# Kernel tuning notes

Measured on AMD Instinct MI355X. Metric: run time of the kernel, lower is better.

Reference implementation:

```python
import jax, jax.numpy as jnp
import numpy as np

B, S, D, F, H, E = 4, 1024, 512, 2048, 8, 8
LN_EPS = 1e-5


def setup_inputs() -> dict:
    key = jax.random.key(0)
    ks = jax.random.split(key, 8)
    sd = 1.0 / np.sqrt(D)
    return {
        'x': jax.random.normal(ks[0], (B, S, D), jnp.float32),
        'in_proj_w': jax.random.normal(ks[1], (3 * D, D), jnp.float32) * sd,
        'in_proj_b': jnp.zeros((3 * D,), jnp.float32),
        'out_proj_w': jax.random.normal(ks[2], (D, D), jnp.float32) * sd,
        'out_proj_b': jnp.zeros((D,), jnp.float32),
        'ln1_g': jnp.ones((D,), jnp.float32),
        'ln1_b': jnp.zeros((D,), jnp.float32),
        'ln2_g': jnp.ones((D,), jnp.float32),
        'ln2_b': jnp.zeros((D,), jnp.float32),
        'router_w': jax.random.normal(ks[3], (D, E), jnp.float32) * sd,
        'wi': jax.random.normal(ks[4], (E, D, F), jnp.float32) * sd,
        'wo': jax.random.normal(ks[5], (E, F, D), jnp.float32) * (1.0 / np.sqrt(F)),
        'expert_capacity': 256,
    }


def _layernorm(x, g, b):
    mu = jnp.mean(x, axis=-1, keepdims=True)
    var = jnp.var(x, axis=-1, keepdims=True)
    return (x - mu) * jax.lax.rsqrt(var + LN_EPS) * g + b


def _mha(x, in_w, in_b, out_w, out_b):
    # torch nn.MultiheadAttention, batch_first, self-attention, no mask
    qkv = x @ in_w.T + in_b                         # [B,S,3D]
    q, k, v = jnp.split(qkv, 3, axis=-1)
    hd = D // H

    def heads(t):
        return t.reshape(B, S, H, hd).transpose(0, 2, 1, 3)  # [B,H,S,hd]

    q, k, v = heads(q), heads(k), heads(v)
    scores = jnp.einsum('bhqd,bhkd->bhqk', q, k) / np.sqrt(hd)
    attn = jax.nn.softmax(scores, axis=-1)
    o = jnp.einsum('bhqk,bhkd->bhqd', attn, v)
    o = o.transpose(0, 2, 1, 3).reshape(B, S, D)
    return o @ out_w.T + out_b


def _router(x, router_w, capacity):
    # Switch-style top-1 router with per-(batch,expert) capacity
    logits = x.astype(jnp.float32) @ router_w       # [B,S,E]
    probs = jax.nn.softmax(logits, axis=-1)
    idx = jnp.argmax(probs, axis=-1)                # [B,S]
    one_hot = jax.nn.one_hot(idx, E, dtype=probs.dtype)
    pos = jnp.cumsum(one_hot, axis=1)               # position within each expert queue
    keep = one_hot * (pos <= capacity).astype(probs.dtype)
    expert_mask = keep * probs                      # dispatch mask scaled by router prob
    return expert_mask, probs, logits


def reference(x, in_proj_w, in_proj_b, out_proj_w, out_proj_b,
              ln1_g, ln1_b, ln2_g, ln2_b, router_w, wi, wo, expert_capacity):
    # self-attention block (post-norm)
    residual = x
    a = _mha(x, in_proj_w, in_proj_b, out_proj_w, out_proj_b)
    h = _layernorm(residual + a, ln1_g, ln1_b)

    # sparse MoE FFN
    expert_mask, _, router_logits = _router(h, router_w, expert_capacity)
    residual = h
    moe = jnp.zeros_like(h)
    for e in range(E):  # fixed small expert loop; masked-dense == gather/FFN/scatter
        y = jax.nn.gelu(h @ wi[e], approximate=False) @ wo[e]
        moe = moe + expert_mask[..., e:e + 1] * y

    out = _layernorm(residual + moe, ln2_g, ln2_b)
    return out, router_logits, expert_mask
```

## Files before the change

### kernel.cpp

```cpp
#include <hip/hip_runtime.h>
#include <math.h>

#define SEQ 1024
#define NTOK 4096
#define DM 512
#define FF 2048
#define NE 8

typedef __attribute__((ext_vector_type(8))) short bf16x8;
typedef __attribute__((ext_vector_type(4))) float f32x4;

__device__ __forceinline__ short f2bf(float f) {
  unsigned u = __float_as_uint(f);
  unsigned r = (u + 0x7FFFu + ((u >> 16) & 1u)) >> 16;
  return (short)r;
}
__device__ __forceinline__ float bf2f(short h) {
  return __uint_as_float(((unsigned)(unsigned short)h) << 16);
}

#define GLOAD_LDS16(g, l) __builtin_amdgcn_global_load_lds( \
    (const __attribute__((address_space(1))) void*)(g),     \
    (__attribute__((address_space(3))) void*)(l), 16, 0, 0)

__global__ __launch_bounds__(256) void split3_kernel(
    const float* __restrict__ x, short* __restrict__ xh, short* __restrict__ xl,
    const float* __restrict__ w1, short* __restrict__ w1h, short* __restrict__ w1l,
    const float* __restrict__ w2, short* __restrict__ w2h, short* __restrict__ w2l) {
  const int bid = blockIdx.x;
  const float* src; short* hi; short* lo; size_t off;
  if (bid < 1024)      { src = x;  hi = xh;  lo = xl;  off = (size_t)bid * 2048; }
  else if (bid < 1408) { src = w1; hi = w1h; lo = w1l; off = (size_t)(bid - 1024) * 2048; }
  else                 { src = w2; hi = w2h; lo = w2l; off = (size_t)(bid - 1408) * 2048; }
  const size_t base = off + threadIdx.x * 8;
  float4 v0 = *reinterpret_cast<const float4*>(src + base);
  float4 v1 = *reinterpret_cast<const float4*>(src + base + 4);
  short h[8]; short l[8];
  float v[8] = {v0.x, v0.y, v0.z, v0.w, v1.x, v1.y, v1.z, v1.w};
#pragma unroll
  for (int i = 0; i < 8; ++i) {
    h[i] = f2bf(v[i]);
    l[i] = f2bf(v[i] - bf2f(h[i]));
  }
  *reinterpret_cast<short4*>(hi + base)     = make_short4(h[0], h[1], h[2], h[3]);
  *reinterpret_cast<short4*>(hi + base + 4) = make_short4(h[4], h[5], h[6], h[7]);
  *reinterpret_cast<short4*>(lo + base)     = make_short4(l[0], l[1], l[2], l[3]);
  *reinterpret_cast<short4*>(lo + base + 4) = make_short4(l[4], l[5], l[6], l[7]);
}

template<int BNF>
__global__ __launch_bounds__(256) void gemm_split(const short* __restrict__ Ah, const short* __restrict__ Al,
    const short* __restrict__ Bh, const short* __restrict__ Bl,
    const float* __restrict__ bias, const float* __restrict__ resid, float* __restrict__ C,
    int N, int K) {
  constexpr int BN = 32 * BNF;
  __shared__ __align__(16) short AsH[128 * 32];
  __shared__ __align__(16) short AsL[128 * 32];
  __shared__ __align__(16) short BsH[BN * 32];
  __shared__ __align__(16) short BsL[BN * 32];
  const int n0 = blockIdx.x * BN, m0 = blockIdx.y * 128;
  const int tid = threadIdx.x;
  const int lane = tid & 63, w = tid >> 6;
  const int quad = lane >> 4, l15 = lane & 15;
  const int wm = (w & 1) * 64, wn = (w >> 1) * 16 * BNF;
  const int sr = tid >> 2, sc = (tid & 3) * 8;
  const short* Ahp = Ah + (size_t)(m0 + sr) * K;
  const short* Alp = Al + (size_t)(m0 + sr) * K;
  const short* Bhp = Bh + (size_t)(n0 + sr) * K;
  const short* Blp = Bl + (size_t)(n0 + sr) * K;
  f32x4 acc[4][BNF];
#pragma unroll
  for (int i = 0; i < 4; ++i)
#pragma unroll
    for (int j = 0; j < BNF; ++j) acc[i][j] = (f32x4){0.f, 0.f, 0.f, 0.f};
  for (int kt = 0; kt < K; kt += 32) {
    GLOAD_LDS16(Ahp + kt + sc,                  &AsH[tid * 8]);
    GLOAD_LDS16(Ahp + (size_t)64 * K + kt + sc, &AsH[2048 + tid * 8]);
    GLOAD_LDS16(Alp + kt + sc,                  &AsL[tid * 8]);
    GLOAD_LDS16(Alp + (size_t)64 * K + kt + sc, &AsL[2048 + tid * 8]);
    if (BNF >= 2 || tid < 128) {
      GLOAD_LDS16(Bhp + kt + sc,                &BsH[tid * 8]);
      GLOAD_LDS16(Blp + kt + sc,                &BsL[tid * 8]);
    }
    if (BNF == 4) {
      GLOAD_LDS16(Bhp + (size_t)64 * K + kt + sc, &BsH[2048 + tid * 8]);
      GLOAD_LDS16(Blp + (size_t)64 * K + kt + sc, &BsL[2048 + tid * 8]);
    }
    __syncthreads();
    bf16x8 ah[4], al[4], bh[BNF], bl[BNF];
#pragma unroll
    for (int i = 0; i < 4; ++i) {
      ah[i] = *reinterpret_cast<const bf16x8*>(&AsH[(wm + i * 16 + l15) * 32 + quad * 8]);
      al[i] = *reinterpret_cast<const bf16x8*>(&AsL[(wm + i * 16 + l15) * 32 + quad * 8]);
    }
#pragma unroll
    for (int j = 0; j < BNF; ++j) {
      bh[j] = *reinterpret_cast<const bf16x8*>(&BsH[(wn + j * 16 + l15) * 32 + quad * 8]);
      bl[j] = *reinterpret_cast<const bf16x8*>(&BsL[(wn + j * 16 + l15) * 32 + quad * 8]);
    }
#pragma unroll
    for (int i = 0; i < 4; ++i)
#pragma unroll
      for (int j = 0; j < BNF; ++j) {
        acc[i][j] = __builtin_amdgcn_mfma_f32_16x16x32_bf16(al[i], bh[j], acc[i][j], 0, 0, 0);
        acc[i][j] = __builtin_amdgcn_mfma_f32_16x16x32_bf16(ah[i], bl[j], acc[i][j], 0, 0, 0);
        acc[i][j] = __builtin_amdgcn_mfma_f32_16x16x32_bf16(ah[i], bh[j], acc[i][j], 0, 0, 0);
      }
    __syncthreads();
  }
#pragma unroll
  for (int i = 0; i < 4; ++i) {
#pragma unroll
    for (int reg = 0; reg < 4; ++reg) {
      const int row = m0 + wm + i * 16 + quad * 4 + reg;
#pragma unroll
      for (int j = 0; j < BNF; ++j) {
        const int col = n0 + wn + j * 16 + l15;
        float v = acc[i][j][reg] + bias[col];
        if (resid) v += resid[(size_t)row * N + col];
        C[(size_t)row * N + col] = v;
      }
    }
  }
}

__global__ __launch_bounds__(256) void gemm_split_qkv(const short* __restrict__ Ah, const short* __restrict__ Al,
    const short* __restrict__ Bh, const short* __restrict__ Bl, const float* __restrict__ bias,
    short* __restrict__ qkh, short* __restrict__ qkl, short* __restrict__ vh, short* __restrict__ vl) {
  const int K = DM;
  __shared__ __align__(16) short AsH[128 * 32];
  __shared__ __align__(16) short AsL[128 * 32];
  __shared__ __align__(16) short BsH[64 * 32];
  __shared__ __align__(16) short BsL[64 * 32];
  const int n0 = blockIdx.x * 64, m0 = blockIdx.y * 128;
  const int tid = threadIdx.x;
  const int lane = tid & 63, w = tid >> 6;
  const int quad = lane >> 4, l15 = lane & 15;
  const int wm = (w & 1) * 64, wn = (w >> 1) * 32;
  const int sr = tid >> 2, sc = (tid & 3) * 8;
  const short* Ahp = Ah + (size_t)(m0 + sr) * K;
  const short* Alp = Al + (size_t)(m0 + sr) * K;
  const short* Bhp = Bh + (size_t)(n0 + sr) * K;
  const short* Blp = Bl + (size_t)(n0 + sr) * K;
  f32x4 acc[4][2];
#pragma unroll
  for (int i = 0; i < 4; ++i)
#pragma unroll
    for (int j = 0; j < 2; ++j) acc[i][j] = (f32x4){0.f, 0.f, 0.f, 0.f};
  for (int kt = 0; kt < K; kt += 32) {
    GLOAD_LDS16(Ahp + kt + sc,                  &AsH[tid * 8]);
    GLOAD_LDS16(Ahp + (size_t)64 * K + kt + sc, &AsH[2048 + tid * 8]);
    GLOAD_LDS16(Alp + kt + sc,                  &AsL[tid * 8]);
    GLOAD_LDS16(Alp + (size_t)64 * K + kt + sc, &AsL[2048 + tid * 8]);
    GLOAD_LDS16(Bhp + kt + sc,                  &BsH[tid * 8]);
    GLOAD_LDS16(Blp + kt + sc,                  &BsL[tid * 8]);
    __syncthreads();
    bf16x8 ah[4], al[4], bh[2], bl[2];
#pragma unroll
    for (int i = 0; i < 4; ++i) {
      ah[i] = *reinterpret_cast<const bf16x8*>(&AsH[(wm + i * 16 + l15) * 32 + quad * 8]);
      al[i] = *reinterpret_cast<const bf16x8*>(&AsL[(wm + i * 16 + l15) * 32 + quad * 8]);
    }
#pragma unroll
    for (int j = 0; j < 2; ++j) {
      bh[j] = *reinterpret_cast<const bf16x8*>(&BsH[(wn + j * 16 + l15) * 32 + quad * 8]);
      bl[j] = *reinterpret_cast<const bf16x8*>(&BsL[(wn + j * 16 + l15) * 32 + quad * 8]);
    }
#pragma unroll
    for (int i = 0; i < 4; ++i)
#pragma unroll
      for (int j = 0; j < 2; ++j) {
        acc[i][j] = __builtin_amdgcn_mfma_f32_16x16x32_bf16(al[i], bh[j], acc[i][j], 0, 0, 0);
        acc[i][j] = __builtin_amdgcn_mfma_f32_16x16x32_bf16(ah[i], bl[j], acc[i][j], 0, 0, 0);
        acc[i][j] = __builtin_amdgcn_mfma_f32_16x16x32_bf16(ah[i], bh[j], acc[i][j], 0, 0, 0);
      }
    __syncthreads();
  }
  if (n0 < 1024) {
#pragma unroll
    for (int i = 0; i < 4; ++i) {
#pragma unroll
      for (int reg = 0; reg < 4; ++reg) {
        const int row = m0 + wm + i * 16 + quad * 4 + reg;
#pragma unroll
        for (int j = 0; j < 2; ++j) {
          const int col = n0 + wn + j * 16 + l15;
          float v = acc[i][j][reg] + bias[col];
          short hv = f2bf(v);
          size_t ad = (size_t)row * 1024 + col;
          qkh[ad] = hv;
          qkl[ad] = f2bf(v - bf2f(hv));
        }
      }
    }
  } else {
#pragma unroll
    for (int i = 0; i < 4; ++i) {
      const int row0 = m0 + wm + i * 16 + quad * 4;
      const int bb = row0 >> 10, s0 = row0 & 1023;
#pragma unroll
      for (int j = 0; j < 2; ++j) {
        const int col = n0 + wn + j * 16 + l15;
        const int c2 = col - 1024;
        const int hhd = c2 >> 6, d = c2 & 63;
        const float bc = bias[col];
        float v0 = acc[i][j][0] + bc, v1 = acc[i][j][1] + bc, v2 = acc[i][j][2] + bc, v3 = acc[i][j][3] + bc;
        short4 hv = make_short4(f2bf(v0), f2bf(v1), f2bf(v2), f2bf(v3));
        short4 lv = make_short4(f2bf(v0 - bf2f(hv.x)), f2bf(v1 - bf2f(hv.y)),
                                f2bf(v2 - bf2f(hv.z)), f2bf(v3 - bf2f(hv.w)));
        size_t ad = ((size_t)(bb * 8 + hhd) * 64 + d) * 1024 + s0;
        *reinterpret_cast<short4*>(vh + ad) = hv;
        *reinterpret_cast<short4*>(vl + ad) = lv;
      }
    }
  }
}

__global__ __launch_bounds__(256) void attn_mfma(const short* __restrict__ qkh, const short* __restrict__ qkl,
    const short* __restrict__ vth, const short* __restrict__ vtl,
    float* __restrict__ opart, float* __restrict__ ml) {
  const int qt = blockIdx.x, hh = blockIdx.y;
  const int b = blockIdx.z >> 1, ks = blockIdx.z & 1;
  __shared__ __align__(16) short Kh[4096], Kl[4096], Vh[4096], Vl[4096];
  const int tid = threadIdx.x;
  const int lane = tid & 63, w = tid >> 6;
  const int quad = lane >> 4, l15 = lane & 15;
  const int tok0 = b * SEQ + qt * 64;
  const int srow = tid >> 2, schunk = (tid & 3) * 8;
  bf16x8 qfh[2], qfl[2];
  {
    const size_t qa = (size_t)(tok0 + w * 16 + l15) * 1024 + hh * 64 + quad * 8;
    qfh[0] = *reinterpret_cast<const bf16x8*>(qkh + qa);
    qfh[1] = *reinterpret_cast<const bf16x8*>(qkh + qa + 32);
    qfl[0] = *reinterpret_cast<const bf16x8*>(qkl + qa);
    qfl[1] = *reinterpret_cast<const bf16x8*>(qkl + qa + 32);
  }
  f32x4 oacc[4];
  float m_run[4], l_run[4];
#pragma unroll
  for (int r = 0; r < 4; ++r) { oacc[r] = (f32x4){0.f, 0.f, 0.f, 0.f}; m_run[r] = -1e30f; l_run[r] = 0.f; }
  const size_t kbase = (size_t)(b * SEQ) * 1024 + 512 + hh * 64;
  const size_t vbase = (size_t)(b * 8 + hh) * 64 * 1024;
  for (int kc = ks * 8; kc < ks * 8 + 8; ++kc) {
    const size_t ka = kbase + (size_t)(kc * 64 + srow) * 1024 + schunk;
    GLOAD_LDS16(qkh + ka,      &Kh[tid * 8]);
    GLOAD_LDS16(qkh + ka + 32, &Kh[2048 + tid * 8]);
    GLOAD_LDS16(qkl + ka,      &Kl[tid * 8]);
    GLOAD_LDS16(qkl + ka + 32, &Kl[2048 + tid * 8]);
    const size_t va = vbase + (size_t)srow * 1024 + kc * 64 + schunk;
    GLOAD_LDS16(vth + va,      &Vh[tid * 8]);
    GLOAD_LDS16(vth + va + 32, &Vh[2048 + tid * 8]);
    GLOAD_LDS16(vtl + va,      &Vl[tid * 8]);
    GLOAD_LDS16(vtl + va + 32, &Vl[2048 + tid * 8]);
    __syncthreads();
    f32x4 s[4];
#pragma unroll
    for (int j = 0; j < 4; ++j) s[j] = (f32x4){0.f, 0.f, 0.f, 0.f};
#pragma unroll
    for (int kk = 0; kk < 2; ++kk)
#pragma unroll
      for (int j = 0; j < 4; ++j) {
        bf16x8 kfh = *reinterpret_cast<const bf16x8*>(&Kh[kk * 2048 + (j * 16 + l15) * 32 + quad * 8]);
        bf16x8 kfl = *reinterpret_cast<const bf16x8*>(&Kl[kk * 2048 + (j * 16 + l15) * 32 + quad * 8]);
        s[j] = __builtin_amdgcn_mfma_f32_16x16x32_bf16(qfl[kk], kfh, s[j], 0, 0, 0);
        s[j] = __builtin_amdgcn_mfma_f32_16x16x32_bf16(qfh[kk], kfl, s[j], 0, 0, 0);
        s[j] = __builtin_amdgcn_mfma_f32_16x16x32_bf16(qfh[kk], kfh, s[j], 0, 0, 0);
      }
    __syncthreads();
    float pv[4][4], alpha[4];
#pragma unroll
    for (int reg = 0; reg < 4; ++reg) {
      float mc = fmaxf(fmaxf(s[0][reg], s[1][reg]), fmaxf(s[2][reg], s[3][reg]));
#pragma unroll
      for (int msk = 1; msk < 16; msk <<= 1) mc = fmaxf(mc, __shfl_xor(mc, msk, 64));
      mc *= 0.125f;
      float mn = fmaxf(m_run[reg], mc);
      alpha[reg] = expf(m_run[reg] - mn);
      m_run[reg] = mn;
      float pl = 0.f;
#pragma unroll
      for (int j = 0; j < 4; ++j) { float pp = expf(s[j][reg] * 0.125f - mn); pv[j][reg] = pp; pl += pp; }
#pragma unroll
      for (int msk = 1; msk < 16; msk <<= 1) pl += __shfl_xor(pl, msk, 64);
      l_run[reg] = l_run[reg] * alpha[reg] + pl;
    }
#pragma unroll
    for (int j = 0; j < 4; ++j) {
      oacc[j][0] *= alpha[0]; oacc[j][1] *= alpha[1]; oacc[j][2] *= alpha[2]; oacc[j][3] *= alpha[3];
    }
#pragma unroll
    for (int j = 0; j < 4; ++j) {
      const int cad = (j >> 1) * 2048 + (j & 1) * 16 + l15;
#pragma unroll
      for (int reg = 0; reg < 4; ++reg) {
        const int ad = cad + (w * 16 + quad * 4 + reg) * 32;
        float p = pv[j][reg];
        short hp = f2bf(p);
        Kh[ad] = hp;
        Kl[ad] = f2bf(p - bf2f(hp));
      }
    }
#pragma unroll
    for (int kk = 0; kk < 2; ++kk) {
      bf16x8 pfh = *reinterpret_cast<const bf16x8*>(&Kh[kk * 2048 + (w * 16 + l15) * 32 + quad * 8]);
      bf16x8 pfl = *reinterpret_cast<const bf16x8*>(&Kl[kk * 2048 + (w * 16 + l15) * 32 + quad * 8]);
#pragma unroll
      for (int j = 0; j < 4; ++j) {
        bf16x8 vfh = *reinterpret_cast<const bf16x8*>(&Vh[kk * 2048 + (j * 16 + l15) * 32 + quad * 8]);
        bf16x8 vfl = *reinterpret_cast<const bf16x8*>(&Vl[kk * 2048 + (j * 16 + l15) * 32 + quad * 8]);
        oacc[j] = __builtin_amdgcn_mfma_f32_16x16x32_bf16(pfl, vfh, oacc[j], 0, 0, 0);
        oacc[j] = __builtin_amdgcn_mfma_f32_16x16x32_bf16(pfh, vfl, oacc[j], 0, 0, 0);
        oacc[j] = __builtin_amdgcn_mfma_f32_16x16x32_bf16(pfh, vfh, oacc[j], 0, 0, 0);
      }
    }
    __syncthreads();
  }
  float* op = opart + (size_t)ks * 2097152;
#pragma unroll
  for (int reg = 0; reg < 4; ++reg) {
    const int rloc = w * 16 + quad * 4 + reg;
#pragma unroll
    for (int j = 0; j < 4; ++j)
      op[(size_t)(tok0 + rloc) * 512 + hh * 64 + j * 16 + l15] = oacc[j][reg];
    if (l15 == 0) {
      size_t mli = (((size_t)ks * 32 + b * 8 + hh) * 1024 + qt * 64 + rloc) * 2;
      ml[mli] = m_run[reg];
      ml[mli + 1] = l_run[reg];
    }
  }
}

__global__ __launch_bounds__(64) void combine_attn(const float* __restrict__ opart, const float* __restrict__ ml,
    short* __restrict__ oh, short* __restrict__ ol) {
  const int t = blockIdx.x;
  const int b = t >> 10, s = t & 1023;
  const int tid = threadIdx.x;
#pragma unroll
  for (int hh = 0; hh < 8; ++hh) {
    size_t mli = (((size_t)(b * 8 + hh)) * 1024 + s) * 2;
    float m0 = ml[mli], l0 = ml[mli + 1];
    float m1 = ml[65536 + mli], l1 = ml[65536 + mli + 1];
    float mm = fmaxf(m0, m1);
    float a0 = expf(m0 - mm), a1 = expf(m1 - mm);
    float inv = 1.f / (l0 * a0 + l1 * a1);
    size_t ad = (size_t)t * 512 + hh * 64 + tid;
    float v = (opart[ad] * a0 + opart[2097152 + ad] * a1) * inv;
    short hv = f2bf(v);
    oh[ad] = hv;
    ol[ad] = f2bf(v - bf2f(hv));
  }
}

__global__ __launch_bounds__(64) void ln_router(const float* __restrict__ r1,
    const float* __restrict__ g, const float* __restrict__ bta, const float* __restrict__ rw,
    float* __restrict__ h, float* __restrict__ rlog, float* __restrict__ probs, int* __restrict__ am) {
  const int t = blockIdx.x, tid = threadIdx.x;
  const size_t base = (size_t)t * DM + tid * 8;
  float4 v0 = *reinterpret_cast<const float4*>(r1 + base);
  float4 v1 = *reinterpret_cast<const float4*>(r1 + base + 4);
  float s = v0.x+v0.y+v0.z+v0.w + v1.x+v1.y+v1.z+v1.w;
  float q = v0.x*v0.x+v0.y*v0.y+v0.z*v0.z+v0.w*v0.w + v1.x*v1.x+v1.y*v1.y+v1.z*v1.z+v1.w*v1.w;
#pragma unroll
  for (int m = 1; m < 64; m <<= 1) { s += __shfl_xor(s, m, 64); q += __shfl_xor(q, m, 64); }
  float mean = s * (1.0f/512.0f);
  float var = q * (1.0f/512.0f) - mean * mean;
  float rs = rsqrtf(var + 1e-5f);
  float4 g0 = *reinterpret_cast<const float4*>(g + tid*8);
  float4 g1 = *reinterpret_cast<const float4*>(g + tid*8 + 4);
  float4 b0 = *reinterpret_cast<const float4*>(bta + tid*8);
  float4 b1 = *reinterpret_cast<const float4*>(bta + tid*8 + 4);
  float hv[8];
  hv[0] = (v0.x-mean)*rs*g0.x+b0.x; hv[1] = (v0.y-mean)*rs*g0.y+b0.y;
  hv[2] = (v0.z-mean)*rs*g0.z+b0.z; hv[3] = (v0.w-mean)*rs*g0.w+b0.w;
  hv[4] = (v1.x-mean)*rs*g1.x+b1.x; hv[5] = (v1.y-mean)*rs*g1.y+b1.y;
  hv[6] = (v1.z-mean)*rs*g1.z+b1.z; hv[7] = (v1.w-mean)*rs*g1.w+b1.w;
  *reinterpret_cast<float4*>(h + base)     = make_float4(hv[0], hv[1], hv[2], hv[3]);
  *reinterpret_cast<float4*>(h + base + 4) = make_float4(hv[4], hv[5], hv[6], hv[7]);
  float lg[8] = {0.f,0.f,0.f,0.f,0.f,0.f,0.f,0.f};
  const float* rwp = rw + tid * 64;
#pragma unroll
  for (int r = 0; r < 8; ++r) {
    float4 w0 = *reinterpret_cast<const float4*>(rwp + r * 8);
    float4 w1 = *reinterpret_cast<const float4*>(rwp + r * 8 + 4);
    float hr = hv[r];
    lg[0] += hr * w0.x; lg[1] += hr * w0.y; lg[2] += hr * w0.z; lg[3] += hr * w0.w;
    lg[4] += hr * w1.x; lg[5] += hr * w1.y; lg[6] += hr * w1.z; lg[7] += hr * w1.w;
  }
#pragma unroll
  for (int m = 1; m < 64; m <<= 1) {
#pragma unroll
    for (int e = 0; e < 8; ++e) lg[e] += __shfl_xor(lg[e], m, 64);
  }
  int best = 0; float bv = lg[0];
#pragma unroll
  for (int e = 1; e < 8; ++e) if (lg[e] > bv) { bv = lg[e]; best = e; }
  float se = 0.f;
#pragma unroll
  for (int e = 0; e < 8; ++e) se += expf(lg[e] - bv);
  float inv = 1.f / se;
  if (tid < 8) {
    rlog[t * 8 + tid] = lg[tid];
    probs[t * 8 + tid] = expf(lg[tid] - bv) * inv;
  }
  if (tid == 0) am[t] = best;
}

__global__ __launch_bounds__(64) void ln2_kernel(const float* __restrict__ x, const float* __restrict__ add,
    const int* __restrict__ pos, const int* __restrict__ capp,
    const float* __restrict__ g, const float* __restrict__ bta, float* __restrict__ y) {
  const int t = blockIdx.x, tid = threadIdx.x;
  const size_t base = (size_t)t * DM + tid * 8;
  float4 v0 = *reinterpret_cast<const float4*>(x + base);
  float4 v1 = *reinterpret_cast<const float4*>(x + base + 4);
  if (pos[t] <= *capp) {
    float4 a0 = *reinterpret_cast<const float4*>(add + base);
    float4 a1 = *reinterpret_cast<const float4*>(add + base + 4);
    v0.x += a0.x; v0.y += a0.y; v0.z += a0.z; v0.w += a0.w;
    v1.x += a1.x; v1.y += a1.y; v1.z += a1.z; v1.w += a1.w;
  }
  float s = v0.x+v0.y+v0.z+v0.w + v1.x+v1.y+v1.z+v1.w;
  float q = v0.x*v0.x+v0.y*v0.y+v0.z*v0.z+v0.w*v0.w + v1.x*v1.x+v1.y*v1.y+v1.z*v1.z+v1.w*v1.w;
#pragma unroll
  for (int m = 1; m < 64; m <<= 1) { s += __shfl_xor(s, m, 64); q += __shfl_xor(q, m, 64); }
  float mean = s * (1.0f/512.0f);
  float var = q * (1.0f/512.0f) - mean * mean;
  float rs = rsqrtf(var + 1e-5f);
  float4 g0 = *reinterpret_cast<const float4*>(g + tid*8);
  float4 g1 = *reinterpret_cast<const float4*>(g + tid*8 + 4);
  float4 b0 = *reinterpret_cast<const float4*>(bta + tid*8);
  float4 b1 = *reinterpret_cast<const float4*>(bta + tid*8 + 4);
  float4 o0 = make_float4((v0.x-mean)*rs*g0.x+b0.x, (v0.y-mean)*rs*g0.y+b0.y,
                          (v0.z-mean)*rs*g0.z+b0.z, (v0.w-mean)*rs*g0.w+b0.w);
  float4 o1 = make_float4((v1.x-mean)*rs*g1.x+b1.x, (v1.y-mean)*rs*g1.y+b1.y,
                          (v1.z-mean)*rs*g1.z+b1.z, (v1.w-mean)*rs*g1.w+b1.w);
  *reinterpret_cast<float4*>(y + base) = o0;
  *reinterpret_cast<float4*>(y + base + 4) = o1;
}

__global__ __launch_bounds__(256) void scan_kernel(const int* __restrict__ am, const float* __restrict__ probs,
    const int* __restrict__ capp, float* __restrict__ emask, int* __restrict__ pos, int* __restrict__ cnt) {
  const int bx = blockIdx.x;
  const int b = bx >> 3, e = bx & 7;
  const int tid = threadIdx.x;
  const int cap = *capp;
  __shared__ int arr[256];
  const int s_base = tid * 4;
  int f[4], incl[4];
  int c = 0;
#pragma unroll
  for (int i = 0; i < 4; ++i) {
    f[i] = (am[b * SEQ + s_base + i] == e) ? 1 : 0;
    c += f[i]; incl[i] = c;
  }
  arr[tid] = c;
  __syncthreads();
  for (int off = 1; off < 256; off <<= 1) {
    int v = (tid >= off) ? arr[tid - off] : 0;
    __syncthreads();
    arr[tid] += v;
    __syncthreads();
  }
  int excl = arr[tid] - c;
  int tot = arr[255];
#pragma unroll
  for (int i = 0; i < 4; ++i) {
    int token = b * SEQ + s_base + i;
    int p = excl + incl[i];
    bool kept = f[i] && (p <= cap);
    emask[(size_t)token * NE + e] = kept ? probs[token * NE + e] : 0.f;
    if (f[i]) pos[token] = p;
  }
  if (tid == 0) cnt[bx] = (tot < cap) ? tot : cap;
}

__global__ __launch_bounds__(256) void transpose2_bf16(const float* __restrict__ wi, short* __restrict__ wi_t,
    const float* __restrict__ wo, short* __restrict__ wo_t) {
  __shared__ float T[32][33];
  const int z = blockIdx.z;
  const float* W; short* Wt; int K, N, k0, n0;
  if (z < 8) { W = wi + (size_t)z * DM * FF;      Wt = wi_t + (size_t)z * DM * FF;
               K = DM; N = FF; k0 = blockIdx.y * 32; n0 = blockIdx.x * 32; }
  else       { W = wo + (size_t)(z - 8) * FF * DM; Wt = wo_t + (size_t)(z - 8) * FF * DM;
               K = FF; N = DM; k0 = blockIdx.x * 32; n0 = blockIdx.y * 32; }
  const int r = threadIdx.x >> 3, c4 = (threadIdx.x & 7) * 4;
  float4 v = *reinterpret_cast<const float4*>(&W[(size_t)(k0 + r) * N + n0 + c4]);
  T[r][c4+0] = v.x; T[r][c4+1] = v.y; T[r][c4+2] = v.z; T[r][c4+3] = v.w;
  __syncthreads();
  short4 o;
  o.x = f2bf(T[c4+0][r]); o.y = f2bf(T[c4+1][r]); o.z = f2bf(T[c4+2][r]); o.w = f2bf(T[c4+3][r]);
  *reinterpret_cast<short4*>(&Wt[(size_t)(n0 + r) * K + k0 + c4]) = o;
}

__global__ __launch_bounds__(128) void gather_kernel(const float* __restrict__ h, const int* __restrict__ am,
    const int* __restrict__ pos, const int* __restrict__ capp, const int* __restrict__ cnt,
    const float* __restrict__ probs, short* __restrict__ Gb, int* __restrict__ tok, float* __restrict__ mscale) {
  const int t = blockIdx.x;
  const int b = t >> 10;
  const int e = am[t];
  const int p = pos[t];
  if (p > *capp) return;
  int off = 0;
  for (int b2 = 0; b2 < b; ++b2) off += cnt[b2 * 8 + e];
  const int slot = off + p - 1;
  const int idx = e * 1024 + slot;
  if (threadIdx.x == 0) { tok[idx] = t; mscale[idx] = probs[t * NE + e]; }
  float4 v = *reinterpret_cast<const float4*>(h + (size_t)t * DM + threadIdx.x * 4);
  short4 o; o.x = f2bf(v.x); o.y = f2bf(v.y); o.z = f2bf(v.z); o.w = f2bf(v.w);
  *reinterpret_cast<short4*>(Gb + (size_t)idx * DM + threadIdx.x * 4) = o;
}

__global__ __launch_bounds__(256) void ffn1_mfma(const short* __restrict__ Gb, const short* __restrict__ wi_t,
    short* __restrict__ mid, const int* __restrict__ cnt) {
  const int e = blockIdx.z;
  const int tot = cnt[e] + cnt[8 + e] + cnt[16 + e] + cnt[24 + e];
  const int m0 = blockIdx.y * 128;
  if (m0 >= tot) return;
  const int n0 = blockIdx.x * 128;
  __shared__ __align__(16) short As[128 * 32];
  __shared__ __align__(16) short Bs[128 * 32];
  const short* A = Gb + ((size_t)e * 1024 + m0) * DM;
  const short* B = wi_t + (size_t)e * FF * DM + (size_t)n0 * DM;
  const int tid = threadIdx.x;
  const int lane = tid & 63, w = tid >> 6;
  const int quad = lane >> 4, l15 = lane & 15;
  const int wm = (w & 1) * 64, wn = (w >> 1) * 64;
  const int sr = tid >> 2, sc = (tid & 3) * 8;
  f32x4 acc[4][4];
#pragma unroll
  for (int i = 0; i < 4; ++i)
#pragma unroll
    for (int j = 0; j < 4; ++j) acc[i][j] = (f32x4){0.f, 0.f, 0.f, 0.f};
  for (int kt = 0; kt < DM; kt += 32) {
    GLOAD_LDS16(A + (size_t)sr * DM + kt + sc,        &As[tid * 8]);
    GLOAD_LDS16(A + (size_t)(sr + 64) * DM + kt + sc, &As[2048 + tid * 8]);
    GLOAD_LDS16(B + (size_t)sr * DM + kt + sc,        &Bs[tid * 8]);
    GLOAD_LDS16(B + (size_t)(sr + 64) * DM + kt + sc, &Bs[2048 + tid * 8]);
    __syncthreads();
    bf16x8 a[4], b[4];
#pragma unroll
    for (int i = 0; i < 4; ++i) a[i] = *reinterpret_cast<const bf16x8*>(&As[(wm + i * 16 + l15) * 32 + quad * 8]);
#pragma unroll
    for (int j = 0; j < 4; ++j) b[j] = *reinterpret_cast<const bf16x8*>(&Bs[(wn + j * 16 + l15) * 32 + quad * 8]);
#pragma unroll
    for (int i = 0; i < 4; ++i)
#pragma unroll
      for (int j = 0; j < 4; ++j)
        acc[i][j] = __builtin_amdgcn_mfma_f32_16x16x32_bf16(a[i], b[j], acc[i][j], 0, 0, 0);
    __syncthreads();
  }
#pragma unroll
  for (int i = 0; i < 4; ++i) {
#pragma unroll
    for (int reg = 0; reg < 4; ++reg) {
      int row = m0 + wm + i * 16 + quad * 4 + reg;
      short* outr = mid + ((size_t)e * 1024 + row) * FF;
#pragma unroll
      for (int j = 0; j < 4; ++j) {
        float v = acc[i][j][reg];
        float gl = 0.5f * v * (1.f + erff(v * 0.70710678118654752f));
        outr[n0 + wn + j * 16 + l15] = f2bf(gl);
      }
    }
  }
}

__global__ __launch_bounds__(256) void ffn2_mfma(const short* __restrict__ mid, const short* __restrict__ wo_t,
    const int* __restrict__ tok, const float* __restrict__ mscale, const int* __restrict__ cnt,
    float* __restrict__ moebuf) {
  const int e = blockIdx.z;
  const int tot = cnt[e] + cnt[8 + e] + cnt[16 + e] + cnt[24 + e];
  const int m0 = blockIdx.y * 128;
  if (m0 >= tot) return;
  const int n0 = blockIdx.x * 64;
  __shared__ __align__(16) short As[128 * 32];
  __shared__ __align__(16) short Bs[64 * 32];
  const short* A = mid + ((size_t)e * 1024 + m0) * FF;
  const short* B = wo_t + (size_t)e * DM * FF + (size_t)n0 * FF;
  const int tid = threadIdx.x;
  const int lane = tid & 63, w = tid >> 6;
  const int quad = lane >> 4, l15 = lane & 15;
  const int wm = (w & 1) * 64, wn = (w >> 1) * 32;
  const int sr = tid >> 2, sc = (tid & 3) * 8;
  f32x4 acc[4][2];
#pragma unroll
  for (int i = 0; i < 4; ++i)
#pragma unroll
    for (int j = 0; j < 2; ++j) acc[i][j] = (f32x4){0.f, 0.f, 0.f, 0.f};
  for (int kt = 0; kt < FF; kt += 32) {
    GLOAD_LDS16(A + (size_t)sr * FF + kt + sc,        &As[tid * 8]);
    GLOAD_LDS16(A + (size_t)(sr + 64) * FF + kt + sc, &As[2048 + tid * 8]);
    GLOAD_LDS16(B + (size_t)sr * FF + kt + sc,        &Bs[tid * 8]);
    __syncthreads();
    bf16x8 a[4], b[2];
#pragma unroll
    for (int i = 0; i < 4; ++i) a[i] = *reinterpret_cast<const bf16x8*>(&As[(wm + i * 16 + l15) * 32 + quad * 8]);
#pragma unroll
    for (int j = 0; j < 2; ++j) b[j] = *reinterpret_cast<const bf16x8*>(&Bs[(wn + j * 16 + l15) * 32 + quad * 8]);
#pragma unroll
    for (int i = 0; i < 4; ++i)
#pragma unroll
      for (int j = 0; j < 2; ++j)
        acc[i][j] = __builtin_amdgcn_mfma_f32_16x16x32_bf16(a[i], b[j], acc[i][j], 0, 0, 0);
    __syncthreads();
  }
#pragma unroll
  for (int i = 0; i < 4; ++i) {
#pragma unroll
    for (int reg = 0; reg < 4; ++reg) {
      int slot = m0 + wm + i * 16 + quad * 4 + reg;
      if (slot < tot) {
        int idx = e * 1024 + slot;
        int t = tok[idx];
        float scv = mscale[idx];
        float* outr = moebuf + (size_t)t * DM + n0 + wn;
#pragma unroll
        for (int j = 0; j < 2; ++j) outr[j * 16 + l15] = scv * acc[i][j][reg];
      }
    }
  }
}

extern "C" void kernel_launch(void* const* d_in, const int* in_sizes, int n_in,
                              void* d_out, int out_size, void* d_ws, size_t ws_size,
                              hipStream_t stream) {
  const float* x     = (const float*)d_in[0];
  const float* in_w  = (const float*)d_in[1];
  const float* in_b  = (const float*)d_in[2];
  const float* out_w = (const float*)d_in[3];
  const float* out_b = (const float*)d_in[4];
  const float* ln1g  = (const float*)d_in[5];
  const float* ln1b  = (const float*)d_in[6];
  const float* ln2g  = (const float*)d_in[7];
  const float* ln2b  = (const float*)d_in[8];
  const float* rw    = (const float*)d_in[9];
  const float* wi    = (const float*)d_in[10];
  const float* wo    = (const float*)d_in[11];
  const int*   capp  = (const int*)d_in[12];

  float* ws = (float*)d_ws;
  short* qkh  = (short*)ws;
  short* qkl  = (short*)(ws + 2097152);
  short* vth  = (short*)(ws + 4194304);
  short* vtl  = (short*)(ws + 5242880);
  short* Gb16 = (short*)ws;
  short* wi_t = (short*)(ws + 2097152);
  float* moebuf = ws + 6291456;
  float* r1     = ws + 8388608;
  float* h      = ws + 10485760;
  float* probs  = ws + 12582912;
  short* wo_t   = (short*)(ws + 12615680);
  float* opart  = ws + 16809984;
  float* mlbuf  = ws + 16809984 + 4194304;
  short* mid16  = (short*)(ws + 16809984);
  float* mscale = ws + 25198592;
  int* am    = (int*)(ws + 25206784);
  int* pos   = am + NTOK;
  int* cnt   = pos + NTOK;
  int* tok   = cnt + 32;
  short* sAh = (short*)(ws + 25231360);
  short* sAl = sAh + 2097152;
  short* sBh = sAl + 2097152;
  short* sBl = sBh + 786432;
  short* sCh = sBl + 786432;
  short* sCl = sCh + 262144;

  float* out   = (float*)d_out;
  float* rlog  = out + 2097152;
  float* emask = rlog + 32768;

  split3_kernel<<<1536, 256, 0, stream>>>(x, sAh, sAl, in_w, sBh, sBl, out_w, sCh, sCl);
  gemm_split_qkv<<<dim3(24, 32), 256, 0, stream>>>(sAh, sAl, sBh, sBl, in_b, qkh, qkl, vth, vtl);
  attn_mfma<<<dim3(16, 8, 8), 256, 0, stream>>>(qkh, qkl, vth, vtl, opart, mlbuf);
  combine_attn<<<NTOK, 64, 0, stream>>>(opart, mlbuf, sAh, sAl);
  gemm_split<1><<<dim3(16, 32), 256, 0, stream>>>(sAh, sAl, sCh, sCl, out_b, x, r1, DM, DM);
  transpose2_bf16<<<dim3(64, 16, 16), 256, 0, stream>>>(wi, wi_t, wo, wo_t);
  ln_router<<<NTOK, 64, 0, stream>>>(r1, ln1g, ln1b, rw, h, rlog, probs, am);
  scan_kernel<<<32, 256, 0, stream>>>(am, probs, capp, emask, pos, cnt);
  gather_kernel<<<NTOK, 128, 0, stream>>>(h, am, pos, capp, cnt, probs, Gb16, tok, mscale);
  ffn1_mfma<<<dim3(16, 8, 8), 256, 0, stream>>>(Gb16, wi_t, mid16, cnt);
  ffn2_mfma<<<dim3(8, 8, 8), 256, 0, stream>>>(mid16, wo_t, tok, mscale, cnt, moebuf);
  ln2_kernel<<<NTOK, 64, 0, stream>>>(h, moebuf, pos, capp, ln2g, ln2b, out);
}
```

Measured before the change: 349.2 us.

## Double-buffer LDS tiles and shrink M-tiles in all GEMM kernels

Converts the QKV, out-projection and both MoE FFN GEMMs to a double-buffered LDS pipeline. The next K-slice is prefetched with global_load_lds while the current one feeds the MFMAs, leaving one barrier per iteration. M-tiles drop from 128 to 64 rows, which doubles the grid to fill more CUs and skips more empty expert slots. The cost is less operand reuse per block, more global traffic, and double the LDS footprint.

```diff
diff --git a/kernel.cpp b/kernel.cpp
--- a/kernel.cpp
+++ b/kernel.cpp
@@ -48,60 +48,52 @@
   *reinterpret_cast<short4*>(lo + base + 4) = make_short4(l[4], l[5], l[6], l[7]);
 }
 
-template<int BNF>
-__global__ __launch_bounds__(256) void gemm_split(const short* __restrict__ Ah, const short* __restrict__ Al,
+__global__ __launch_bounds__(256) void gemm_split_db(const short* __restrict__ Ah, const short* __restrict__ Al,
     const short* __restrict__ Bh, const short* __restrict__ Bl,
     const float* __restrict__ bias, const float* __restrict__ resid, float* __restrict__ C,
     int N, int K) {
-  constexpr int BN = 32 * BNF;
-  __shared__ __align__(16) short AsH[128 * 32];
-  __shared__ __align__(16) short AsL[128 * 32];
-  __shared__ __align__(16) short BsH[BN * 32];
-  __shared__ __align__(16) short BsL[BN * 32];
-  const int n0 = blockIdx.x * BN, m0 = blockIdx.y * 128;
+  __shared__ __align__(16) short AsH[2][2048], AsL[2][2048], BsH[2][2048], BsL[2][2048];
+  const int n0 = blockIdx.x * 64, m0 = blockIdx.y * 64;
   const int tid = threadIdx.x;
   const int lane = tid & 63, w = tid >> 6;
   const int quad = lane >> 4, l15 = lane & 15;
-  const int wm = (w & 1) * 64, wn = (w >> 1) * 16 * BNF;
+  const int wm = (w & 1) * 32, wn = (w >> 1) * 32;
   const int sr = tid >> 2, sc = (tid & 3) * 8;
-  const short* Ahp = Ah + (size_t)(m0 + sr) * K;
-  const short* Alp = Al + (size_t)(m0 + sr) * K;
-  const short* Bhp = Bh + (size_t)(n0 + sr) * K;
-  const short* Blp = Bl + (size_t)(n0 + sr) * K;
-  f32x4 acc[4][BNF];
-#pragma unroll
-  for (int i = 0; i < 4; ++i)
-#pragma unroll
-    for (int j = 0; j < BNF; ++j) acc[i][j] = (f32x4){0.f, 0.f, 0.f, 0.f};
+  const short* Ahp = Ah + (size_t)(m0 + sr) * K + sc;
+  const short* Alp = Al + (size_t)(m0 + sr) * K + sc;
+  const short* Bhp = Bh + (size_t)(n0 + sr) * K + sc;
+  const short* Blp = Bl + (size_t)(n0 + sr) * K + sc;
+  GLOAD_LDS16(Ahp, &AsH[0][tid * 8]);
+  GLOAD_LDS16(Alp, &AsL[0][tid * 8]);
+  GLOAD_LDS16(Bhp, &BsH[0][tid * 8]);
+  GLOAD_LDS16(Blp, &BsL[0][tid * 8]);
+  __syncthreads();
+  f32x4 acc[2][2];
+#pragma unroll
+  for (int i = 0; i < 2; ++i)
+#pragma unroll
+    for (int j = 0; j < 2; ++j) acc[i][j] = (f32x4){0.f, 0.f, 0.f, 0.f};
   for (int kt = 0; kt < K; kt += 32) {
-    GLOAD_LDS16(Ahp + kt + sc,                  &AsH[tid * 8]);
-    GLOAD_LDS16(Ahp + (size_t)64 * K + kt + sc, &AsH[2048 + tid * 8]);
-    GLOAD_LDS16(Alp + kt + sc,                  &AsL[tid * 8]);
-    GLOAD_LDS16(Alp + (size_t)64 * K + kt + sc, &AsL[2048 + tid * 8]);
-    if (BNF >= 2 || tid < 128) {
-      GLOAD_LDS16(Bhp + kt + sc,                &BsH[tid * 8]);
-      GLOAD_LDS16(Blp + kt + sc,                &BsL[tid * 8]);
-    }
-    if (BNF == 4) {
-      GLOAD_LDS16(Bhp + (size_t)64 * K + kt + sc, &BsH[2048 + tid * 8]);
-      GLOAD_LDS16(Blp + (size_t)64 * K + kt + sc, &BsL[2048 + tid * 8]);
-    }
-    __syncthreads();
-    bf16x8 ah[4], al[4], bh[BNF], bl[BNF];
-#pragma unroll
-    for (int i = 0; i < 4; ++i) {
-      ah[i] = *reinterpret_cast<const bf16x8*>(&AsH[(wm + i * 16 + l15) * 32 + quad * 8]);
-      al[i] = *reinterpret_cast<const bf16x8*>(&AsL[(wm + i * 16 + l15) * 32 + quad * 8]);
-    }
-#pragma unroll
-    for (int j = 0; j < BNF; ++j) {
-      bh[j] = *reinterpret_cast<const bf16x8*>(&BsH[(wn + j * 16 + l15) * 32 + quad * 8]);
-      bl[j] = *reinterpret_cast<const bf16x8*>(&BsL[(wn + j * 16 + l15) * 32 + quad * 8]);
-    }
-#pragma unroll
-    for (int i = 0; i < 4; ++i)
-#pragma unroll
-      for (int j = 0; j < BNF; ++j) {
+    const int cur = (kt >> 5) & 1;
+    if (kt + 32 < K) {
+      const int nxt = cur ^ 1;
+      GLOAD_LDS16(Ahp + kt + 32, &AsH[nxt][tid * 8]);
+      GLOAD_LDS16(Alp + kt + 32, &AsL[nxt][tid * 8]);
+      GLOAD_LDS16(Bhp + kt + 32, &BsH[nxt][tid * 8]);
+      GLOAD_LDS16(Blp + kt + 32, &BsL[nxt][tid * 8]);
+    }
+    bf16x8 ah[2], al[2], bh[2], bl[2];
+#pragma unroll
+    for (int i = 0; i < 2; ++i) {
+      ah[i] = *reinterpret_cast<const bf16x8*>(&AsH[cur][(wm + i * 16 + l15) * 32 + quad * 8]);
+      al[i] = *reinterpret_cast<const bf16x8*>(&AsL[cur][(wm + i * 16 + l15) * 32 + quad * 8]);
+      bh[i] = *reinterpret_cast<const bf16x8*>(&BsH[cur][(wn + i * 16 + l15) * 32 + quad * 8]);
+      bl[i] = *reinterpret_cast<const bf16x8*>(&BsL[cur][(wn + i * 16 + l15) * 32 + quad * 8]);
+    }
+#pragma unroll
+    for (int i = 0; i < 2; ++i)
+#pragma unroll
+      for (int j = 0; j < 2; ++j) {
         acc[i][j] = __builtin_amdgcn_mfma_f32_16x16x32_bf16(al[i], bh[j], acc[i][j], 0, 0, 0);
         acc[i][j] = __builtin_amdgcn_mfma_f32_16x16x32_bf16(ah[i], bl[j], acc[i][j], 0, 0, 0);
         acc[i][j] = __builtin_amdgcn_mfma_f32_16x16x32_bf16(ah[i], bh[j], acc[i][j], 0, 0, 0);
@@ -109,15 +101,14 @@
     __syncthreads();
   }
 #pragma unroll
-  for (int i = 0; i < 4; ++i) {
+  for (int i = 0; i < 2; ++i) {
 #pragma unroll
     for (int reg = 0; reg < 4; ++reg) {
       const int row = m0 + wm + i * 16 + quad * 4 + reg;
 #pragma unroll
-      for (int j = 0; j < BNF; ++j) {
+      for (int j = 0; j < 2; ++j) {
         const int col = n0 + wn + j * 16 + l15;
-        float v = acc[i][j][reg] + bias[col];
-        if (resid) v += resid[(size_t)row * N + col];
+        float v = acc[i][j][reg] + bias[col] + resid[(size_t)row * N + col];
         C[(size_t)row * N + col] = v;
       }
     }
@@ -128,46 +119,46 @@
     const short* __restrict__ Bh, const short* __restrict__ Bl, const float* __restrict__ bias,
     short* __restrict__ qkh, short* __restrict__ qkl, short* __restrict__ vh, short* __restrict__ vl) {
   const int K = DM;
-  __shared__ __align__(16) short AsH[128 * 32];
-  __shared__ __align__(16) short AsL[128 * 32];
-  __shared__ __align__(16) short BsH[64 * 32];
-  __shared__ __align__(16) short BsL[64 * 32];
-  const int n0 = blockIdx.x * 64, m0 = blockIdx.y * 128;
+  __shared__ __align__(16) short AsH[2][2048], AsL[2][2048], BsH[2][2048], BsL[2][2048];
+  const int n0 = blockIdx.x * 64, m0 = blockIdx.y * 64;
   const int tid = threadIdx.x;
   const int lane = tid & 63, w = tid >> 6;
   const int quad = lane >> 4, l15 = lane & 15;
-  const int wm = (w & 1) * 64, wn = (w >> 1) * 32;
+  const int wm = (w & 1) * 32, wn = (w >> 1) * 32;
   const int sr = tid >> 2, sc = (tid & 3) * 8;
-  const short* Ahp = Ah + (size_t)(m0 + sr) * K;
-  const short* Alp = Al + (size_t)(m0 + sr) * K;
-  const short* Bhp = Bh + (size_t)(n0 + sr) * K;
-  const short* Blp = Bl + (size_t)(n0 + sr) * K;
-  f32x4 acc[4][2];
-#pragma unroll
-  for (int i = 0; i < 4; ++i)
+  const short* Ahp = Ah + (size_t)(m0 + sr) * K + sc;
+  const short* Alp = Al + (size_t)(m0 + sr) * K + sc;
+  const short* Bhp = Bh + (size_t)(n0 + sr) * K + sc;
+  const short* Blp = Bl + (size_t)(n0 + sr) * K + sc;
+  GLOAD_LDS16(Ahp, &AsH[0][tid * 8]);
+  GLOAD_LDS16(Alp, &AsL[0][tid * 8]);
+  GLOAD_LDS16(Bhp, &BsH[0][tid * 8]);
+  GLOAD_LDS16(Blp, &BsL[0][tid * 8]);
+  __syncthreads();
+  f32x4 acc[2][2];
+#pragma unroll
+  for (int i = 0; i < 2; ++i)
 #pragma unroll
     for (int j = 0; j < 2; ++j) acc[i][j] = (f32x4){0.f, 0.f, 0.f, 0.f};
   for (int kt = 0; kt < K; kt += 32) {
-    GLOAD_LDS16(Ahp + kt + sc,                  &AsH[tid * 8]);
-    GLOAD_LDS16(Ahp + (size_t)64 * K + kt + sc, &AsH[2048 + tid * 8]);
-    GLOAD_LDS16(Alp + kt + sc,                  &AsL[tid * 8]);
-    GLOAD_LDS16(Alp + (size_t)64 * K + kt + sc, &AsL[2048 + tid * 8]);
-    GLOAD_LDS16(Bhp + kt + sc,                  &BsH[tid * 8]);
-    GLOAD_LDS16(Blp + kt + sc,                  &BsL[tid * 8]);
-    __syncthreads();
-    bf16x8 ah[4], al[4], bh[2], bl[2];
-#pragma unroll
-    for (int i = 0; i < 4; ++i) {
-      ah[i] = *reinterpret_cast<const bf16x8*>(&AsH[(wm + i * 16 + l15) * 32 + quad * 8]);
-      al[i] = *reinterpret_cast<const bf16x8*>(&AsL[(wm + i * 16 + l15) * 32 + quad * 8]);
-    }
-#pragma unroll
-    for (int j = 0; j < 2; ++j) {
-      bh[j] = *reinterpret_cast<const bf16x8*>(&BsH[(wn + j * 16 + l15) * 32 + quad * 8]);
-      bl[j] = *reinterpret_cast<const bf16x8*>(&BsL[(wn + j * 16 + l15) * 32 + quad * 8]);
-    }
-#pragma unroll
-    for (int i = 0; i < 4; ++i)
+    const int cur = (kt >> 5) & 1;
+    if (kt + 32 < K) {
+      const int nxt = cur ^ 1;
+      GLOAD_LDS16(Ahp + kt + 32, &AsH[nxt][tid * 8]);
+      GLOAD_LDS16(Alp + kt + 32, &AsL[nxt][tid * 8]);
+      GLOAD_LDS16(Bhp + kt + 32, &BsH[nxt][tid * 8]);
+      GLOAD_LDS16(Blp + kt + 32, &BsL[nxt][tid * 8]);
+    }
+    bf16x8 ah[2], al[2], bh[2], bl[2];
+#pragma unroll
+    for (int i = 0; i < 2; ++i) {
+      ah[i] = *reinterpret_cast<const bf16x8*>(&AsH[cur][(wm + i * 16 + l15) * 32 + quad * 8]);
+      al[i] = *reinterpret_cast<const bf16x8*>(&AsL[cur][(wm + i * 16 + l15) * 32 + quad * 8]);
+      bh[i] = *reinterpret_cast<const bf16x8*>(&BsH[cur][(wn + i * 16 + l15) * 32 + quad * 8]);
+      bl[i] = *reinterpret_cast<const bf16x8*>(&BsL[cur][(wn + i * 16 + l15) * 32 + quad * 8]);
+    }
+#pragma unroll
+    for (int i = 0; i < 2; ++i)
 #pragma unroll
       for (int j = 0; j < 2; ++j) {
         acc[i][j] = __builtin_amdgcn_mfma_f32_16x16x32_bf16(al[i], bh[j], acc[i][j], 0, 0, 0);
@@ -178,7 +169,7 @@
   }
   if (n0 < 1024) {
 #pragma unroll
-    for (int i = 0; i < 4; ++i) {
+    for (int i = 0; i < 2; ++i) {
 #pragma unroll
       for (int reg = 0; reg < 4; ++reg) {
         const int row = m0 + wm + i * 16 + quad * 4 + reg;
@@ -195,7 +186,7 @@
     }
   } else {
 #pragma unroll
-    for (int i = 0; i < 4; ++i) {
+    for (int i = 0; i < 2; ++i) {
       const int row0 = m0 + wm + i * 16 + quad * 4;
       const int bb = row0 >> 10, s0 = row0 & 1023;
 #pragma unroll
@@ -513,38 +504,45 @@
     short* __restrict__ mid, const int* __restrict__ cnt) {
   const int e = blockIdx.z;
   const int tot = cnt[e] + cnt[8 + e] + cnt[16 + e] + cnt[24 + e];
-  const int m0 = blockIdx.y * 128;
+  const int m0 = blockIdx.y * 64;
   if (m0 >= tot) return;
   const int n0 = blockIdx.x * 128;
-  __shared__ __align__(16) short As[128 * 32];
-  __shared__ __align__(16) short Bs[128 * 32];
-  const short* A = Gb + ((size_t)e * 1024 + m0) * DM;
-  const short* B = wi_t + (size_t)e * FF * DM + (size_t)n0 * DM;
+  __shared__ __align__(16) short As[2][2048];
+  __shared__ __align__(16) short Bs[2][4096];
   const int tid = threadIdx.x;
   const int lane = tid & 63, w = tid >> 6;
   const int quad = lane >> 4, l15 = lane & 15;
-  const int wm = (w & 1) * 64, wn = (w >> 1) * 64;
+  const int wn = w * 32;
   const int sr = tid >> 2, sc = (tid & 3) * 8;
-  f32x4 acc[4][4];
+  const short* Ap  = Gb + ((size_t)e * 1024 + m0 + sr) * DM + sc;
+  const short* Bp  = wi_t + (size_t)e * FF * DM + (size_t)(n0 + sr) * DM + sc;
+  const short* Bp2 = wi_t + (size_t)e * FF * DM + (size_t)(n0 + 64 + sr) * DM + sc;
+  GLOAD_LDS16(Ap,  &As[0][tid * 8]);
+  GLOAD_LDS16(Bp,  &Bs[0][tid * 8]);
+  GLOAD_LDS16(Bp2, &Bs[0][2048 + tid * 8]);
+  __syncthreads();
+  f32x4 acc[4][2];
 #pragma unroll
   for (int i = 0; i < 4; ++i)
 #pragma unroll
-    for (int j = 0; j < 4; ++j) acc[i][j] = (f32x4){0.f, 0.f, 0.f, 0.f};
+    for (int j = 0; j < 2; ++j) acc[i][j] = (f32x4){0.f, 0.f, 0.f, 0.f};
   for (int kt = 0; kt < DM; kt += 32) {
-    GLOAD_LDS16(A + (size_t)sr * DM + kt + sc,        &As[tid * 8]);
-    GLOAD_LDS16(A + (size_t)(sr + 64) * DM + kt + sc, &As[2048 + tid * 8]);
-    GLOAD_LDS16(B + (size_t)sr * DM + kt + sc,        &Bs[tid * 8]);
-    GLOAD_LDS16(B + (size_t)(sr + 64) * DM + kt + sc, &Bs[2048 + tid * 8]);
-    __syncthreads();
-    bf16x8 a[4], b[4];
-#pragma unroll
-    for (int i = 0; i < 4; ++i) a[i] = *reinterpret_cast<const bf16x8*>(&As[(wm + i * 16 + l15) * 32 + quad * 8]);
-#pragma unroll
-    for (int j = 0; j < 4; ++j) b[j] = *reinterpret_cast<const bf16x8*>(&Bs[(wn + j * 16 + l15) * 32 + quad * 8]);
+    const int cur = (kt >> 5) & 1;
+    if (kt + 32 < DM) {
+      const int nxt = cur ^ 1;
+      GLOAD_LDS16(Ap + kt + 32,  &As[nxt][tid * 8]);
+      GLOAD_LDS16(Bp + kt + 32,  &Bs[nxt][tid * 8]);
+      GLOAD_LDS16(Bp2 + kt + 32, &Bs[nxt][2048 + tid * 8]);
+    }
+    bf16x8 a[4], b[2];
+#pragma unroll
+    for (int i = 0; i < 4; ++i) a[i] = *reinterpret_cast<const bf16x8*>(&As[cur][(i * 16 + l15) * 32 + quad * 8]);
+#pragma unroll
+    for (int j = 0; j < 2; ++j) b[j] = *reinterpret_cast<const bf16x8*>(&Bs[cur][(wn + j * 16 + l15) * 32 + quad * 8]);
 #pragma unroll
     for (int i = 0; i < 4; ++i)
 #pragma unroll
-      for (int j = 0; j < 4; ++j)
+      for (int j = 0; j < 2; ++j)
         acc[i][j] = __builtin_amdgcn_mfma_f32_16x16x32_bf16(a[i], b[j], acc[i][j], 0, 0, 0);
     __syncthreads();
   }
@@ -552,10 +550,10 @@
   for (int i = 0; i < 4; ++i) {
 #pragma unroll
     for (int reg = 0; reg < 4; ++reg) {
-      int row = m0 + wm + i * 16 + quad * 4 + reg;
+      const int row = m0 + i * 16 + quad * 4 + reg;
       short* outr = mid + ((size_t)e * 1024 + row) * FF;
 #pragma unroll
-      for (int j = 0; j < 4; ++j) {
+      for (int j = 0; j < 2; ++j) {
         float v = acc[i][j][reg];
         float gl = 0.5f * v * (1.f + erff(v * 0.70710678118654752f));
         outr[n0 + wn + j * 16 + l15] = f2bf(gl);
@@ -569,49 +567,55 @@
     float* __restrict__ moebuf) {
   const int e = blockIdx.z;
   const int tot = cnt[e] + cnt[8 + e] + cnt[16 + e] + cnt[24 + e];
-  const int m0 = blockIdx.y * 128;
+  const int m0 = blockIdx.y * 64;
   if (m0 >= tot) return;
   const int n0 = blockIdx.x * 64;
-  __shared__ __align__(16) short As[128 * 32];
-  __shared__ __align__(16) short Bs[64 * 32];
-  const short* A = mid + ((size_t)e * 1024 + m0) * FF;
-  const short* B = wo_t + (size_t)e * DM * FF + (size_t)n0 * FF;
+  __shared__ __align__(16) short As[2][2048];
+  __shared__ __align__(16) short Bs[2][2048];
   const int tid = threadIdx.x;
   const int lane = tid & 63, w = tid >> 6;
   const int quad = lane >> 4, l15 = lane & 15;
-  const int wm = (w & 1) * 64, wn = (w >> 1) * 32;
+  const int wm = (w & 1) * 32, wn = (w >> 1) * 32;
   const int sr = tid >> 2, sc = (tid & 3) * 8;
-  f32x4 acc[4][2];
-#pragma unroll
-  for (int i = 0; i < 4; ++i)
+  const short* Ap = mid + ((size_t)e * 1024 + m0 + sr) * FF + sc;
+  const short* Bp = wo_t + (size_t)e * DM * FF + (size_t)(n0 + sr) * FF + sc;
+  GLOAD_LDS16(Ap, &As[0][tid * 8]);
+  GLOAD_LDS16(Bp, &Bs[0][tid * 8]);
+  __syncthreads();
+  f32x4 acc[2][2];
+#pragma unroll
+  for (int i = 0; i < 2; ++i)
 #pragma unroll
     for (int j = 0; j < 2; ++j) acc[i][j] = (f32x4){0.f, 0.f, 0.f, 0.f};
   for (int kt = 0; kt < FF; kt += 32) {
-    GLOAD_LDS16(A + (size_t)sr * FF + kt + sc,        &As[tid * 8]);
-    GLOAD_LDS16(A + (size_t)(sr + 64) * FF + kt + sc, &As[2048 + tid * 8]);
-    GLOAD_LDS16(B + (size_t)sr * FF + kt + sc,        &Bs[tid * 8]);
-    __syncthreads();
-    bf16x8 a[4], b[2];
-#pragma unroll
-    for (int i = 0; i < 4; ++i) a[i] = *reinterpret_cast<const bf16x8*>(&As[(wm + i * 16 + l15) * 32 + quad * 8]);
-#pragma unroll
-    for (int j = 0; j < 2; ++j) b[j] = *reinterpret_cast<const bf16x8*>(&Bs[(wn + j * 16 + l15) * 32 + quad * 8]);
-#pragma unroll
-    for (int i = 0; i < 4; ++i)
+    const int cur = (kt >> 5) & 1;
+    if (kt + 32 < FF) {
+      const int nxt = cur ^ 1;
+      GLOAD_LDS16(Ap + kt + 32, &As[nxt][tid * 8]);
+      GLOAD_LDS16(Bp + kt + 32, &Bs[nxt][tid * 8]);
+    }
+    bf16x8 a[2], b[2];
+#pragma unroll
+    for (int i = 0; i < 2; ++i) {
+      a[i] = *reinterpret_cast<const bf16x8*>(&As[cur][(wm + i * 16 + l15) * 32 + quad * 8]);
+      b[i] = *reinterpret_cast<const bf16x8*>(&Bs[cur][(wn + i * 16 + l15) * 32 + quad * 8]);
+    }
+#pragma unroll
+    for (int i = 0; i < 2; ++i)
 #pragma unroll
       for (int j = 0; j < 2; ++j)
         acc[i][j] = __builtin_amdgcn_mfma_f32_16x16x32_bf16(a[i], b[j], acc[i][j], 0, 0, 0);
     __syncthreads();
   }
 #pragma unroll
-  for (int i = 0; i < 4; ++i) {
+  for (int i = 0; i < 2; ++i) {
 #pragma unroll
     for (int reg = 0; reg < 4; ++reg) {
-      int slot = m0 + wm + i * 16 + quad * 4 + reg;
+      const int slot = m0 + wm + i * 16 + quad * 4 + reg;
       if (slot < tot) {
-        int idx = e * 1024 + slot;
-        int t = tok[idx];
-        float scv = mscale[idx];
+        const int idx = e * 1024 + slot;
+        const int t = tok[idx];
+        const float scv = mscale[idx];
         float* outr = moebuf + (size_t)t * DM + n0 + wn;
 #pragma unroll
         for (int j = 0; j < 2; ++j) outr[j * 16 + l15] = scv * acc[i][j][reg];
@@ -669,15 +673,15 @@
   float* emask = rlog + 32768;
 
   split3_kernel<<<1536, 256, 0, stream>>>(x, sAh, sAl, in_w, sBh, sBl, out_w, sCh, sCl);
-  gemm_split_qkv<<<dim3(24, 32), 256, 0, stream>>>(sAh, sAl, sBh, sBl, in_b, qkh, qkl, vth, vtl);
+  gemm_split_qkv<<<dim3(24, 64), 256, 0, stream>>>(sAh, sAl, sBh, sBl, in_b, qkh, qkl, vth, vtl);
   attn_mfma<<<dim3(16, 8, 8), 256, 0, stream>>>(qkh, qkl, vth, vtl, opart, mlbuf);
   combine_attn<<<NTOK, 64, 0, stream>>>(opart, mlbuf, sAh, sAl);
-  gemm_split<1><<<dim3(16, 32), 256, 0, stream>>>(sAh, sAl, sCh, sCl, out_b, x, r1, DM, DM);
+  gemm_split_db<<<dim3(8, 64), 256, 0, stream>>>(sAh, sAl, sCh, sCl, out_b, x, r1, DM, DM);
   transpose2_bf16<<<dim3(64, 16, 16), 256, 0, stream>>>(wi, wi_t, wo, wo_t);
   ln_router<<<NTOK, 64, 0, stream>>>(r1, ln1g, ln1b, rw, h, rlog, probs, am);
   scan_kernel<<<32, 256, 0, stream>>>(am, probs, capp, emask, pos, cnt);
   gather_kernel<<<NTOK, 128, 0, stream>>>(h, am, pos, capp, cnt, probs, Gb16, tok, mscale);
-  ffn1_mfma<<<dim3(16, 8, 8), 256, 0, stream>>>(Gb16, wi_t, mid16, cnt);
-  ffn2_mfma<<<dim3(8, 8, 8), 256, 0, stream>>>(mid16, wo_t, tok, mscale, cnt, moebuf);
+  ffn1_mfma<<<dim3(16, 16, 8), 256, 0, stream>>>(Gb16, wi_t, mid16, cnt);
+  ffn2_mfma<<<dim3(8, 16, 8), 256, 0, stream>>>(mid16, wo_t, tok, mscale, cnt, moebuf);
   ln2_kernel<<<NTOK, 64, 0, stream>>>(h, moebuf, pos, capp, ln2g, ln2b, out);
 }
```

Measured after the change: 352.1 us. About the same (+0.8%).
